# Performance work log

Measured on AMD Instinct MI355X. Metric: run time of the kernel, lower is better.

Reference implementation:

```python
import jax, jax.numpy as jnp
import numpy as np
import math

B, L_DEC, L_ENC, D, H = 2, 512, 2048, 1024, 16
HD = D // H
SCALE = HD ** -0.5
C = 5
N_TOP = min(L_DEC, max(1, int(C * math.log(L_DEC + 1))))      # 31
N_SAMPLE = min(L_ENC, max(1, int(C * math.log(L_ENC + 1))))   # 38
TAU = 1.0


def setup_inputs() -> dict:
    key = jax.random.key(0)
    ks = jax.random.split(key, 8)
    s = D ** -0.5
    return {
        "decoder_hidden": jax.random.normal(ks[0], (B, L_DEC, D), jnp.float32),
        "encoder_output": jax.random.normal(ks[1], (B, L_ENC, D), jnp.float32),
        "Wq": jax.random.normal(ks[2], (D, D), jnp.float32) * s,
        "Wk": jax.random.normal(ks[3], (D, D), jnp.float32) * s,
        "Wv": jax.random.normal(ks[4], (D, D), jnp.float32) * s,
        "Wo": jax.random.normal(ks[5], (D, D), jnp.float32) * s,
        "rms_w": jnp.ones((D,), jnp.float32),
        "alphas": 0.01 * jax.random.normal(ks[6], (6,), jnp.float32),
        "sample_idx": jax.random.permutation(ks[7], L_ENC)[:N_SAMPLE].astype(jnp.int32),
    }


def _split(x, L):
    # [B,L,D] -> [B,H,L,hd]
    return x.reshape(B, L, H, HD).transpose(0, 2, 1, 3)


def _merge(x):
    # [B,H,L,hd] -> [B,L,D]
    return x.transpose(0, 2, 1, 3).reshape(B, -1, D)


def _rmsnorm(x, w):
    return x * jax.lax.rsqrt(jnp.mean(x * x, axis=-1, keepdims=True) + 1e-6) * w


def _sdp(q, k, v):
    s = jnp.einsum('bhtd,bhsd->bhts', q, k) * SCALE
    return jnp.einsum('bhts,bhsd->bhtd', jax.nn.softmax(s, axis=-1), v)


def _linear(q, k, v):
    qf = jax.nn.elu(q * SCALE) + 1.0
    kf = jax.nn.elu(k) + 1.0
    kv = jnp.einsum('bhsd,bhsv->bhdv', kf, v)
    denom = jnp.maximum(jnp.einsum('bhtd,bhd->bht', qf, kf.sum(axis=2)), 1e-6)
    return jnp.einsum('bhtd,bhdv->bhtv', qf, kv) / denom[..., None]


def _cosine(q, k, v):
    qn = q / jnp.maximum(jnp.linalg.norm(q, axis=-1, keepdims=True), 1e-12)
    kn = k / jnp.maximum(jnp.linalg.norm(k, axis=-1, keepdims=True), 1e-12)
    qf = jax.nn.relu(qn) + 1e-6
    kf = jax.nn.relu(kn) + 1e-6
    kv = jnp.einsum('bhsd,bhsv->bhdv', kf, v)
    denom = jnp.maximum(jnp.einsum('bhtd,bhd->bht', qf, kf.sum(axis=2)), 1e-6)
    return jnp.einsum('bhtd,bhdv->bhtv', qf, kv) / denom[..., None]


def _probsparse(q, k, v, sample_idx):
    ks = k[:, :, sample_idx, :]                              # [B,H,n_sample,hd]
    qs = jnp.einsum('bhtd,bhsd->bhts', q, ks) * SCALE
    M = qs.max(axis=-1) - qs.mean(axis=-1)                   # sparsity score [B,H,T]
    _, top_idx = jax.lax.top_k(M, N_TOP)                     # [B,H,n_top]
    v_mean = v.mean(axis=2, keepdims=True)
    out = jnp.broadcast_to(v_mean, (B, H, L_DEC, HD))
    q_top = jnp.take_along_axis(q, top_idx[..., None], axis=2)
    s_top = jnp.einsum('bhtd,bhsd->bhts', q_top, k) * SCALE
    out_top = jnp.einsum('bhts,bhsd->bhtd', jax.nn.softmax(s_top, axis=-1), v)
    bi = jnp.arange(B)[:, None, None]
    hi = jnp.arange(H)[None, :, None]
    return out.at[bi, hi, top_idx].set(out_top)


def _local(q, k, v):
    W = max(4, int(L_ENC * 0.25))
    dec_pos = jnp.arange(L_DEC, dtype=jnp.float32)
    center = jnp.clip((dec_pos * (L_ENC / max(L_DEC, 1))).astype(jnp.int32), 0, L_ENC - 1)
    half = W // 2
    lo = jnp.clip(center - half, 0, L_ENC - 1)
    hi = jnp.clip(center + half, 0, L_ENC - 1)
    enc_pos = jnp.arange(L_ENC)
    mask = (enc_pos[None, :] >= lo[:, None]) & (enc_pos[None, :] <= hi[:, None])  # [T,S]
    s = jnp.einsum('bhtd,bhsd->bhts', q, k) * SCALE
    s = jnp.where(mask[None, None], s, -jnp.inf)
    attn = jax.nn.softmax(s, axis=-1)
    attn = jnp.where(jnp.isnan(attn), 1.0 / L_ENC, attn)
    return jnp.einsum('bhts,bhsd->bhtd', attn, v)


def _forward(decoder_hidden, encoder_output, Wq, Wk, Wv, Wo, rms_w, alphas, sample_idx):
    q = _split(decoder_hidden @ Wq, L_DEC)
    k = _split(encoder_output @ Wk, L_ENC)
    v = _split(encoder_output @ Wv, L_ENC)
    # MODES order: none, sdp, linear, probsparse, cosine, local
    branches = [_sdp(q, k, v), _linear(q, k, v), _probsparse(q, k, v, sample_idx),
                _cosine(q, k, v), _local(q, k, v)]
    w = jax.nn.softmax(alphas / TAU)
    out = w[0] * decoder_hidden  # 'none' branch is identity passthrough
    for i, raw in enumerate(branches):
        out = out + w[i + 1] * _rmsnorm(decoder_hidden + _merge(raw) @ Wo, rms_w)
    return out


def reference(decoder_hidden, encoder_output, Wq, Wk, Wv, Wo, rms_w, alphas, sample_idx):
    return _forward(decoder_hidden, encoder_output, Wq, Wk, Wv, Wo, rms_w, alphas, sample_idx)
```

## Files before the change

### kernel.cpp

```cpp
#include <hip/hip_runtime.h>
#include <math.h>

#define LDEC 512
#define LENC 2048
#define DMODEL 1024
#define NH 16
#define HD 64
#define SCALE 0.125f
#define NTOP 31
#define NSAMP 38

typedef __attribute__((ext_vector_type(8))) short bf16x8;
typedef __attribute__((ext_vector_type(4))) float f32x4;

__device__ inline float wave_sum(float v) {
#pragma unroll
  for (int m = 32; m > 0; m >>= 1) v += __shfl_xor(v, m);
  return v;
}

__device__ inline unsigned short f2bf(float x) {
  unsigned u = __float_as_uint(x);
  u += 0x7fff + ((u >> 16) & 1);
  return (unsigned short)(u >> 16);
}
__device__ inline float bf2f(unsigned short h) {
  return __uint_as_float(((unsigned)h) << 16);
}

__device__ __forceinline__ void gld16(const unsigned short* g, unsigned short* l) {
  __builtin_amdgcn_global_load_lds(
      (const __attribute__((address_space(1))) unsigned int*)g,
      (__attribute__((address_space(3))) unsigned int*)l, 16, 0, 0);
}

__device__ __forceinline__ int sws(int row, int col) {
  return row * 64 + (col ^ ((row & 7) << 3));
}

__global__ __launch_bounds__(256) void prologue(
    const float* __restrict__ dec, const float* __restrict__ enc,
    const float* __restrict__ Wq, const float* __restrict__ Wk,
    const float* __restrict__ Wv, const int* __restrict__ sidx,
    unsigned short* __restrict__ dh, unsigned short* __restrict__ dl,
    unsigned short* __restrict__ eh,
    unsigned short* __restrict__ Wqh, unsigned short* __restrict__ Wql,
    unsigned short* __restrict__ Wkh, unsigned short* __restrict__ Wvh,
    float* __restrict__ KsPart) {
  extern __shared__ char smraw[];
  int bx = blockIdx.x;
  int tid = threadIdx.x;
  if (bx < 5120) {
    int i = bx * 256 + tid;
    if (i < 262144) {
      float4 v = ((const float4*)dec)[i];
      ushort4 h = make_ushort4(f2bf(v.x), f2bf(v.y), f2bf(v.z), f2bf(v.w));
      ushort4 l = make_ushort4(f2bf(v.x - bf2f(h.x)), f2bf(v.y - bf2f(h.y)),
                               f2bf(v.z - bf2f(h.z)), f2bf(v.w - bf2f(h.w)));
      *(ushort4*)(dh + i * 4) = h;
      *(ushort4*)(dl + i * 4) = l;
    } else {
      int j = i - 262144;
      float4 v = ((const float4*)enc)[j];
      *(ushort4*)(eh + j * 4) =
          make_ushort4(f2bf(v.x), f2bf(v.y), f2bf(v.z), f2bf(v.w));
    }
  } else if (bx < 5888) {
    float (*t)[68] = (float(*)[68])smraw;
    int wb = bx - 5120;
    int which = wb >> 8, rem = wb & 255;
    const float* W = which == 0 ? Wq : (which == 1 ? Wk : Wv);
    unsigned short* Th = which == 0 ? Wqh : (which == 1 ? Wkh : Wvh);
    unsigned short* Tl = which == 0 ? Wql : nullptr;
    int k0 = (rem >> 4) * 64, n0 = (rem & 15) * 64;
#pragma unroll
    for (int i = 0; i < 4; ++i) {
      int c = tid + 256 * i;
      int r = c >> 4, c4 = (c & 15) * 4;
      float4 v = *(const float4*)(W + (size_t)(k0 + r) * DMODEL + n0 + c4);
      t[c4 + 0][r] = v.x; t[c4 + 1][r] = v.y; t[c4 + 2][r] = v.z; t[c4 + 3][r] = v.w;
    }
    __syncthreads();
#pragma unroll
    for (int i = 0; i < 4; ++i) {
      int c = tid + 256 * i;
      int n = c >> 4, k4 = (c & 15) * 4;
      float4 v = *(const float4*)&t[n][k4];
      ushort4 h = make_ushort4(f2bf(v.x), f2bf(v.y), f2bf(v.z), f2bf(v.w));
      *(ushort4*)(Th + (size_t)(n0 + n) * DMODEL + k0 + k4) = h;
      if (Tl) {
        ushort4 l = make_ushort4(f2bf(v.x - bf2f(h.x)), f2bf(v.y - bf2f(h.y)),
                                 f2bf(v.z - bf2f(h.z)), f2bf(v.w - bf2f(h.w)));
        *(ushort4*)(Tl + (size_t)(n0 + n) * DMODEL + k0 + k4) = l;
      }
    }
  } else {
    float* er = (float*)smraw;
    int sb = bx - 5888;
    int s = sb >> 5;
    int rem = sb & 31;
    int cchunk = rem >> 3, kc = rem & 7;
    int c = cchunk * 256 + tid;
    int srow = sidx[s];
    if (tid < 32) {
      int idx = tid * 4;
      *(float4*)&er[idx] =
          *(const float4*)(enc + (size_t)srow * DMODEL + kc * 128 + idx);
    }
    __syncthreads();
    float acc = 0.f;
    const float* wp = Wk + (size_t)(kc * 128) * DMODEL + c;
    for (int k0 = 0; k0 < 128; k0 += 16) {
      float w[16];
#pragma unroll
      for (int j = 0; j < 16; ++j) w[j] = wp[(size_t)(k0 + j) * DMODEL];
#pragma unroll
      for (int j = 0; j < 16; ++j) acc = fmaf(er[k0 + j], w[j], acc);
    }
    KsPart[(size_t)kc * (NSAMP * 1024) + s * 1024 + c] = acc;
  }
}

template <int BF16OUT>
__device__ __forceinline__ void gemm_epilogue(
    unsigned short* sm, f32x4 (&acc)[4][2], float* __restrict__ C,
    unsigned short* __restrict__ Cb, int row0, int col0, int wave, int lane) {
  const int l16 = lane & 15, quad = lane >> 4;
  float* eL = (float*)sm + wave * 576;
  const int rr = lane >> 2, cc = (lane & 3) * 8;
  const int wr = wave >> 2, wc = wave & 3;
#pragma unroll
  for (int x = 0; x < 4; ++x) {
#pragma unroll
    for (int y = 0; y < 2; ++y)
#pragma unroll
      for (int q = 0; q < 4; ++q)
        eL[(quad * 4 + q) * 36 + y * 16 + l16] = acc[x][y][q];
    float4 v0 = *(const float4*)&eL[rr * 36 + cc];
    float4 v1 = *(const float4*)&eL[rr * 36 + cc + 4];
    size_t ro = (size_t)(row0 + wr * 64 + x * 16 + rr) * DMODEL + col0 + wc * 32 + cc;
    if (BF16OUT) {
      uint2 o;
      o.x = (unsigned)f2bf(v0.x) | ((unsigned)f2bf(v0.y) << 16);
      o.y = (unsigned)f2bf(v0.z) | ((unsigned)f2bf(v0.w) << 16);
      *(uint2*)(Cb + ro) = o;
      o.x = (unsigned)f2bf(v1.x) | ((unsigned)f2bf(v1.y) << 16);
      o.y = (unsigned)f2bf(v1.z) | ((unsigned)f2bf(v1.w) << 16);
      *(uint2*)(Cb + ro + 4) = o;
    } else {
      *(float4*)(C + ro) = v0;
      *(float4*)(C + ro + 4) = v1;
    }
  }
}

template <int BF16OUT>
__device__ __forceinline__ void gemm512_1p_async(
    const unsigned short* __restrict__ Ah, const unsigned short* __restrict__ Bh,
    float* __restrict__ C, unsigned short* __restrict__ Cb, int row0, int col0) {
  extern __shared__ unsigned short sm[];
  const int BUFS = 16384;
  const int tid = threadIdx.x, lane = tid & 63, wave = tid >> 6;
  const int l16 = lane & 15, quad = lane >> 4;
  const int wr = wave >> 2, wc = wave & 3;

  const int srow = wave * 16 + (lane >> 3);
  const int scol = ((lane & 7) ^ (lane >> 3)) * 8;
  const unsigned short* gA = Ah + (size_t)(row0 + srow) * DMODEL + scol;
  const unsigned short* gB = Bh + (size_t)(col0 + srow) * DMODEL + scol;
  const int wofs = wave * 1024;

  f32x4 acc[4][2];
#pragma unroll
  for (int x = 0; x < 4; ++x)
#pragma unroll
    for (int y = 0; y < 2; ++y) acc[x][y] = (f32x4){0.f, 0.f, 0.f, 0.f};

  gld16(gA, sm + wofs);
  gld16(gA + (size_t)8 * DMODEL, sm + wofs + 512);
  gld16(gB, sm + 8192 + wofs);
  gld16(gB + (size_t)8 * DMODEL, sm + 8192 + wofs + 512);
  __syncthreads();

  for (int it = 0; it < 16; ++it) {
    const unsigned short* cur = sm + (it & 1) * BUFS;
    if (it < 15) {
      int ko = (it + 1) * 64;
      unsigned short* nxt = sm + ((it + 1) & 1) * BUFS;
      gld16(gA + ko, nxt + wofs);
      gld16(gA + (size_t)8 * DMODEL + ko, nxt + wofs + 512);
      gld16(gB + ko, nxt + 8192 + wofs);
      gld16(gB + (size_t)8 * DMODEL + ko, nxt + 8192 + wofs + 512);
    }
    bf16x8 a[2][4], b[2][2];
#pragma unroll
    for (int ks = 0; ks < 2; ++ks) {
#pragma unroll
      for (int x = 0; x < 4; ++x)
        a[ks][x] = *(const bf16x8*)&cur[sws(wr * 64 + x * 16 + l16, ks * 32 + quad * 8)];
#pragma unroll
      for (int y = 0; y < 2; ++y)
        b[ks][y] = *(const bf16x8*)&cur[8192 + sws(wc * 32 + y * 16 + l16, ks * 32 + quad * 8)];
    }
#pragma unroll
    for (int ks = 0; ks < 2; ++ks)
#pragma unroll
      for (int x = 0; x < 4; ++x)
#pragma unroll
        for (int y = 0; y < 2; ++y)
          acc[x][y] = __builtin_amdgcn_mfma_f32_16x16x32_bf16(a[ks][x], b[ks][y], acc[x][y], 0, 0, 0);
    __syncthreads();
  }
  gemm_epilogue<BF16OUT>(sm, acc, C, Cb, row0, col0, wave, lane);
}

__device__ __forceinline__ void gemm512_3p(
    const unsigned short* __restrict__ Ah, const unsigned short* __restrict__ Al,
    const unsigned short* __restrict__ Bh, const unsigned short* __restrict__ Bl,
    float* __restrict__ C, int row0, int col0) {
  extern __shared__ unsigned short sm[];
  const int BUFS = 20480;
  const int tid = threadIdx.x, lane = tid & 63, wave = tid >> 6;
  const int l16 = lane & 15, quad = lane >> 4;
  const int wr = wave >> 2, wc = wave & 3;

  const int r = tid >> 2, kc = tid & 3;
  const unsigned short* gAh = Ah + (size_t)(row0 + r) * DMODEL + kc * 8;
  const unsigned short* gBh = Bh + (size_t)(col0 + r) * DMODEL + kc * 8;
  const unsigned short* gAl = Al + (size_t)(row0 + r) * DMODEL + kc * 8;
  const unsigned short* gBl = Bl + (size_t)(col0 + r) * DMODEL + kc * 8;
  const int lofs = r * 40 + kc * 8;

  f32x4 acc[4][2];
#pragma unroll
  for (int x = 0; x < 4; ++x)
#pragma unroll
    for (int y = 0; y < 2; ++y) acc[x][y] = (f32x4){0.f, 0.f, 0.f, 0.f};

  uint4 pah = *(const uint4*)gAh, pbh = *(const uint4*)gBh;
  uint4 pal = *(const uint4*)gAl, pbl = *(const uint4*)gBl;
  *(uint4*)&sm[lofs] = pah;
  *(uint4*)&sm[5120 + lofs] = pbh;
  *(uint4*)&sm[10240 + lofs] = pal;
  *(uint4*)&sm[15360 + lofs] = pbl;
  pah = *(const uint4*)(gAh + 32);
  pbh = *(const uint4*)(gBh + 32);
  pal = *(const uint4*)(gAl + 32);
  pbl = *(const uint4*)(gBl + 32);
  __syncthreads();

  for (int it = 0; it < 32; ++it) {
    const unsigned short* cur = sm + (it & 1) * BUFS;
    bf16x8 ah[4], bh[2], al[4], bl[2];
#pragma unroll
    for (int x = 0; x < 4; ++x) {
      ah[x] = *(const bf16x8*)&cur[(wr * 64 + x * 16 + l16) * 40 + quad * 8];
      al[x] = *(const bf16x8*)&cur[10240 + (wr * 64 + x * 16 + l16) * 40 + quad * 8];
    }
#pragma unroll
    for (int y = 0; y < 2; ++y) {
      bh[y] = *(const bf16x8*)&cur[5120 + (wc * 32 + y * 16 + l16) * 40 + quad * 8];
      bl[y] = *(const bf16x8*)&cur[15360 + (wc * 32 + y * 16 + l16) * 40 + quad * 8];
    }
#pragma unroll
    for (int x = 0; x < 4; ++x)
#pragma unroll
      for (int y = 0; y < 2; ++y) {
        acc[x][y] = __builtin_amdgcn_mfma_f32_16x16x32_bf16(ah[x], bh[y], acc[x][y], 0, 0, 0);
        acc[x][y] = __builtin_amdgcn_mfma_f32_16x16x32_bf16(ah[x], bl[y], acc[x][y], 0, 0, 0);
        acc[x][y] = __builtin_amdgcn_mfma_f32_16x16x32_bf16(al[x], bh[y], acc[x][y], 0, 0, 0);
      }
    if (it < 31) {
// ... 99 lines not shown
      const int s0 = ch * 64;
      {
        const unsigned short* kr = Kg + (size_t)(s0 + sK) * DMODEL + d16;
        uint4 p0 = *(const uint4*)kr;
        uint4 p1 = *(const uint4*)(kr + 8);
        float kvv[16];
        kvv[0] = __uint_as_float(p0.x << 16);
        kvv[1] = __uint_as_float(p0.x & 0xffff0000u);
        kvv[2] = __uint_as_float(p0.y << 16);
        kvv[3] = __uint_as_float(p0.y & 0xffff0000u);
        kvv[4] = __uint_as_float(p0.z << 16);
        kvv[5] = __uint_as_float(p0.z & 0xffff0000u);
        kvv[6] = __uint_as_float(p0.w << 16);
        kvv[7] = __uint_as_float(p0.w & 0xffff0000u);
        kvv[8] = __uint_as_float(p1.x << 16);
        kvv[9] = __uint_as_float(p1.x & 0xffff0000u);
        kvv[10] = __uint_as_float(p1.y << 16);
        kvv[11] = __uint_as_float(p1.y & 0xffff0000u);
        kvv[12] = __uint_as_float(p1.z << 16);
        kvv[13] = __uint_as_float(p1.z & 0xffff0000u);
        kvv[14] = __uint_as_float(p1.w << 16);
        kvv[15] = __uint_as_float(p1.w & 0xffff0000u);
        float ss = 0.f;
#pragma unroll
        for (int j = 0; j < 16; ++j) ss = fmaf(kvv[j], kvv[j], ss);
        ss += __shfl_xor(ss, 1);
        ss += __shfl_xor(ss, 2);
        if ((tid & 3) == 0) nrm[sK] = sqrtf(ss);
#pragma unroll
        for (int j = 0; j < 16; ++j) Kt[sK][d16 + j] = kvv[j];
      }
#pragma unroll
      for (int i = 0; i < 4; ++i) {
        int sv = sVb + 16 * i;
        float4 vv = *(const float4*)(Vg + (size_t)(s0 + sv) * DMODEL + v4);
        vpart.x += vv.x; vpart.y += vv.y; vpart.z += vv.z; vpart.w += vv.w;
        unsigned short h0 = f2bf(vv.x), h1 = f2bf(vv.y);
        unsigned short h2 = f2bf(vv.z), h3 = f2bf(vv.w);
        Vu[sv][v4 + 0] = ((unsigned)h0 << 16) | (unsigned)f2bf(vv.x - bf2f(h0));
        Vu[sv][v4 + 1] = ((unsigned)h1 << 16) | (unsigned)f2bf(vv.y - bf2f(h1));
        Vu[sv][v4 + 2] = ((unsigned)h2 << 16) | (unsigned)f2bf(vv.z - bf2f(h2));
        Vu[sv][v4 + 3] = ((unsigned)h3 << 16) | (unsigned)f2bf(vv.w - bf2f(h3));
      }
      __syncthreads();
#pragma unroll
      for (int kk = 0; kk < 2; ++kk) {
        const int sb = kk * 32 + quad * 8;
        bf16x8 aLh, aLl, aCh, aCl;
#pragma unroll
        for (int j = 0; j < 8; ++j) {
          float kval = Kt[sb + j][dblk + l16];
          float nn = nrm[sb + j];
          float kfl = kval > 0.f ? kval + 1.f : __expf(kval);
          float kn = kval / fmaxf(nn, 1e-12f);
          float kfc = fmaxf(kn, 0.f) + 1e-6f;
          kslp += kfl;
          kscp += kfc;
          unsigned short hL = f2bf(kfl);
          aLh[j] = hL;
          aLl[j] = f2bf(kfl - bf2f(hL));
          unsigned short hC = f2bf(kfc);
          aCh[j] = hC;
          aCl[j] = f2bf(kfc - bf2f(hC));
        }
#pragma unroll
        for (int n = 0; n < 4; ++n) {
          bf16x8 bhv, blv;
#pragma unroll
          for (int j = 0; j < 8; ++j) {
            unsigned uv = Vu[sb + j][n * 16 + l16];
            bhv[j] = (short)(unsigned short)(uv >> 16);
            blv[j] = (short)(unsigned short)(uv & 0xffffu);
          }
          accL[n] = __builtin_amdgcn_mfma_f32_16x16x32_bf16(aLh, bhv, accL[n], 0, 0, 0);
          accL[n] = __builtin_amdgcn_mfma_f32_16x16x32_bf16(aLh, blv, accL[n], 0, 0, 0);
          accL[n] = __builtin_amdgcn_mfma_f32_16x16x32_bf16(aLl, bhv, accL[n], 0, 0, 0);
          accC[n] = __builtin_amdgcn_mfma_f32_16x16x32_bf16(aCh, bhv, accC[n], 0, 0, 0);
          accC[n] = __builtin_amdgcn_mfma_f32_16x16x32_bf16(aCh, blv, accC[n], 0, 0, 0);
          accC[n] = __builtin_amdgcn_mfma_f32_16x16x32_bf16(aCl, bhv, accC[n], 0, 0, 0);
        }
      }
      __syncthreads();
    }
    const int obase = part * 131072 + bh * 4096;
#pragma unroll
    for (int n = 0; n < 4; ++n)
#pragma unroll
      for (int q = 0; q < 4; ++q) {
        int o = obase + (dblk + quad * 4 + q) * 64 + n * 16 + l16;
        kvpL[o] = accL[n][q];
        kvpC[o] = accC[n][q];
      }
    kslp += __shfl_xor(kslp, 16);
    kslp += __shfl_xor(kslp, 32);
    kscp += __shfl_xor(kscp, 16);
    kscp += __shfl_xor(kscp, 32);
    if (quad == 0) {
      kspL[part * 2048 + bh * 64 + dblk + l16] = kslp;
      kspC[part * 2048 + bh * 64 + dblk + l16] = kscp;
    }
    vpart.x += __shfl_xor(vpart.x, 16); vpart.x += __shfl_xor(vpart.x, 32);
    vpart.y += __shfl_xor(vpart.y, 16); vpart.y += __shfl_xor(vpart.y, 32);
    vpart.z += __shfl_xor(vpart.z, 16); vpart.z += __shfl_xor(vpart.z, 32);
    vpart.w += __shfl_xor(vpart.w, 16); vpart.w += __shfl_xor(vpart.w, 32);
    if (quad == 0) vred[wv * 16 + l16] = vpart;
    __syncthreads();
    if (tid < 16) {
      float4 a0 = vred[tid], a1 = vred[16 + tid];
      float4 a2 = vred[32 + tid], a3 = vred[48 + tid];
      float4 s = make_float4(a0.x + a1.x + a2.x + a3.x, a0.y + a1.y + a2.y + a3.y,
                             a0.z + a1.z + a2.z + a3.z, a0.w + a1.w + a2.w + a3.w);
      *(float4*)&vsp[part * 2048 + bh * 64 + tid * 4] = s;
    }
  } else {
    float (*ksL)[65] = (float(*)[65])smraw;
    int bx = bx0 - 1536;
    int bh = bx >> 2, chunk = bx & 3;
    int b = bh >> 4, h = bh & 15;
    int t0 = chunk * 128;
    const float* Qb = Q + (b * LDEC) * DMODEL + h * HD;
    for (int slot = tid; slot < NSAMP * 16; slot += 256) {
      int r = slot >> 4, c4 = slot & 15;
      const float* kp = KsPart + r * 1024 + h * HD + c4 * 4;
      float4 kx = *(const float4*)kp;
#pragma unroll
      for (int p = 1; p < 8; ++p) {
        float4 k2 = *(const float4*)(kp + (size_t)p * (NSAMP * 1024));
        kx.x += k2.x; kx.y += k2.y; kx.z += k2.z; kx.w += k2.w;
      }
      ksL[r][c4 * 4 + 0] = kx.x; ksL[r][c4 * 4 + 1] = kx.y;
      ksL[r][c4 * 4 + 2] = kx.z; ksL[r][c4 * 4 + 3] = kx.w;
    }
    __syncthreads();
    if (tid < 128) {
      float qr[64];
      const float* qrow = Qb + (size_t)(t0 + tid) * DMODEL;
#pragma unroll
      for (int d4 = 0; d4 < 16; ++d4)
        *(float4*)&qr[d4 * 4] = *(const float4*)(qrow + d4 * 4);
      float mx = -INFINITY, sm = 0.f;
      for (int j = 0; j < NSAMP; ++j) {
        float s = 0.f;
#pragma unroll
        for (int d = 0; d < 64; ++d) s = fmaf(qr[d], ksL[j][d], s);
        s *= SCALE;
        mx = fmaxf(mx, s);
        sm += s;
      }
      Mout[bh * LDEC + t0 + tid] = mx - sm / (float)NSAMP;
    }
  }
}

__global__ __launch_bounds__(256) void tail2(
    const float* __restrict__ kvpL, const float* __restrict__ kvpC,
    const float* __restrict__ kspL, const float* __restrict__ kspC,
    const float* __restrict__ vsp, float* __restrict__ kvL,
    float* __restrict__ kvC, float* __restrict__ ksL,
    float* __restrict__ ksC, float* __restrict__ vmean,
    const float* __restrict__ Mbuf, int* __restrict__ sel) {
  extern __shared__ char smraw[];
  int bx = blockIdx.x;
  int tid = threadIdx.x;
  if (bx < 1048) {
    int i = bx * 256 + tid;
    if (i < 131072) {
      float s = 0.f;
#pragma unroll
      for (int p = 0; p < 16; ++p) s += kvpL[p * 131072 + i];
      kvL[i] = s;
    } else if (i < 262144) {
      int j = i - 131072;
      float s = 0.f;
#pragma unroll
      for (int p = 0; p < 16; ++p) s += kvpC[p * 131072 + j];
      kvC[j] = s;
    } else if (i < 268288) {
      int j = i - 262144;
      int which = j >> 11, jj = j & 2047;
      const float* src = which == 0 ? kspL : (which == 1 ? kspC : vsp);
      float s = 0.f;
#pragma unroll
      for (int p = 0; p < 16; ++p) s += src[p * 2048 + jj];
      if (which == 0) ksL[jj] = s;
      else if (which == 1) ksC[jj] = s;
      else vmean[jj] = s * (1.f / 2048.f);
    }
  } else {
    float* vals = (float*)smraw;
    int* flag = (int*)(smraw + 2048);
    float* wvs = (float*)(smraw + 4096);
    int* wis = (int*)(smraw + 4112);
    int bh = bx - 1048;
    int lane = tid & 63, g = tid >> 6;
    vals[tid] = Mbuf[bh * 512 + tid];
    vals[tid + 256] = Mbuf[bh * 512 + tid + 256];
    flag[tid] = 0; flag[tid + 256] = 0;
    __syncthreads();
    for (int it = 0; it < NTOP; ++it) {
      float v0 = vals[tid]; int i0 = tid;
      float v1 = vals[tid + 256];
      if (v1 > v0) { v0 = v1; i0 = tid + 256; }
#pragma unroll
      for (int mm = 32; mm > 0; mm >>= 1) {
        float ov = __shfl_xor(v0, mm);
        int oi = __shfl_xor(i0, mm);
        if (ov > v0 || (ov == v0 && oi < i0)) { v0 = ov; i0 = oi; }
      }
      if (lane == 0) { wvs[g] = v0; wis[g] = i0; }
      __syncthreads();
      if (tid == 0) {
        float bv = wvs[0]; int bi = wis[0];
#pragma unroll
        for (int w = 1; w < 4; ++w)
          if (wvs[w] > bv || (wvs[w] == bv && wis[w] < bi)) { bv = wvs[w]; bi = wis[w]; }
        vals[bi] = -INFINITY;
        flag[bi] = 1;
      }
      __syncthreads();
    }
    sel[bh * 512 + tid] = flag[tid];
    sel[bh * 512 + tid + 256] = flag[tid + 256];
  }
}

__global__ __launch_bounds__(256) void attn_mfma(
    const float* __restrict__ Qf, const unsigned short* __restrict__ Kb,
    const unsigned short* __restrict__ Vt,
    float* __restrict__ OsP0, float* __restrict__ OsP1,
    float* __restrict__ OsP2, float* __restrict__ OsP3,
    float* __restrict__ OlS0, float* __restrict__ OlS1,
    float* __restrict__ st) {
  __shared__ unsigned short Ks[2][4096];
  __shared__ unsigned short Vs[2][4096];
  __shared__ unsigned short Ps[4][1024];
  const int tid = threadIdx.x;
  const int wave = tid >> 6, lane = tid & 63;
  const int l16 = lane & 15, quad = lane >> 4;
  const int bx = blockIdx.x;
  const int xcd = bx & 7, sub = bx >> 3;
  const int qt = sub & 7, qr = (sub >> 3) & 3, grp = sub >> 5;
  const int bh = xcd + 8 * grp;
  const int b = bh >> 4, h = bh & 15;
  const int tbase = qt * 64 + wave * 16;
  const int sbase = qr * 512;

  const float* qrow = Qf + (size_t)(b * LDEC + tbase + l16) * DMODEL + h * HD + quad * 8;
  bf16x8 qa0, qa1;
  {
    float4 a0 = *(const float4*)qrow, a1 = *(const float4*)(qrow + 4);
    float4 a2 = *(const float4*)(qrow + 32), a3 = *(const float4*)(qrow + 36);
    qa0[0] = f2bf(a0.x * SCALE); qa0[1] = f2bf(a0.y * SCALE);
    qa0[2] = f2bf(a0.z * SCALE); qa0[3] = f2bf(a0.w * SCALE);
    qa0[4] = f2bf(a1.x * SCALE); qa0[5] = f2bf(a1.y * SCALE);
    qa0[6] = f2bf(a1.z * SCALE); qa0[7] = f2bf(a1.w * SCALE);
    qa1[0] = f2bf(a2.x * SCALE); qa1[1] = f2bf(a2.y * SCALE);
    qa1[2] = f2bf(a2.z * SCALE); qa1[3] = f2bf(a2.w * SCALE);
    qa1[4] = f2bf(a3.x * SCALE); qa1[5] = f2bf(a3.y * SCALE);
    qa1[6] = f2bf(a3.z * SCALE); qa1[7] = f2bf(a3.w * SCALE);
  }

  bf16x8 bone;
#pragma unroll
  for (int j = 0; j < 8; ++j) bone[j] = (short)0x3f80;

  int tA = tbase + l16;
  int cA = min(4 * tA, LENC - 1);
  int loA = max(cA - 256, 0), hiA = min(cA + 256, LENC - 1);
  const int loW = max(4 * tbase - 256, 0);
  const int hiW = min(4 * (tbase + 15) + 256, LENC - 1);
  const bool blockAny = (sbase <= hiW) && (sbase + 511 >= loW);

  f32x4 Os[4], Ol[4], Ssum, Slsum;
#pragma unroll
  for (int n = 0; n < 4; ++n) {
    Os[n] = (f32x4){0.f, 0.f, 0.f, 0.f};
    Ol[n] = (f32x4){0.f, 0.f, 0.f, 0.f};
  }
  Ssum = (f32x4){0.f, 0.f, 0.f, 0.f};
  Slsum = (f32x4){0.f, 0.f, 0.f, 0.f};

  const int c0 = tid, c1 = tid + 256;
  const unsigned short* kg0 = Kb + (size_t)(b * LENC + sbase + (c0 >> 3)) * DMODEL + h * HD + (c0 & 7) * 8;
  const unsigned short* kg1 = Kb + (size_t)(b * LENC + sbase + (c1 >> 3)) * DMODEL + h * HD + (c1 & 7) * 8;
  const unsigned short* vg0 = Vt + (size_t)(bh * 64 + (c0 >> 3)) * LENC + sbase + (c0 & 7) * 8;
  const unsigned short* vg1 = Vt + (size_t)(bh * 64 + (c1 >> 3)) * LENC + sbase + (c1 & 7) * 8;
  const int of0 = sws(c0 >> 3, (c0 & 7) * 8);
  const int of1 = sws(c1 >> 3, (c1 & 7) * 8);

  uint4 pk0, pk1, pv0, pv1;
  pk0 = *(const uint4*)kg0; pk1 = *(const uint4*)kg1;
  pv0 = *(const uint4*)vg0; pv1 = *(const uint4*)vg1;
  *(uint4*)&Ks[0][of0] = pk0; *(uint4*)&Ks[0][of1] = pk1;
  *(uint4*)&Vs[0][of0] = pv0; *(uint4*)&Vs[0][of1] = pv1;
  __syncthreads();

  for (int it = 0; it < 8; ++it) {
    const int cur = it & 1;
    const int s0 = sbase + it * 64;
    const bool anyL = (s0 <= hiW) && (s0 + 63 >= loW);
    if (it < 7) {
      pk0 = *(const uint4*)(kg0 + (size_t)(it + 1) * 64 * DMODEL);
      pk1 = *(const uint4*)(kg1 + (size_t)(it + 1) * 64 * DMODEL);
      pv0 = *(const uint4*)(vg0 + (it + 1) * 64);
      pv1 = *(const uint4*)(vg1 + (it + 1) * 64);
    }
    const unsigned short* K_ = Ks[cur];
    const unsigned short* V_ = Vs[cur];

    f32x4 S[4];
#pragma unroll
    for (int n = 0; n < 4; ++n) {
      bf16x8 bk0 = *(const bf16x8*)&K_[sws(n * 16 + l16, quad * 8)];
      bf16x8 bk1 = *(const bf16x8*)&K_[sws(n * 16 + l16, 32 + quad * 8)];
      f32x4 z = (f32x4){0.f, 0.f, 0.f, 0.f};
      z = __builtin_amdgcn_mfma_f32_16x16x32_bf16(qa0, bk0, z, 0, 0, 0);
      S[n] = __builtin_amdgcn_mfma_f32_16x16x32_bf16(qa1, bk1, z, 0, 0, 0);
    }

    unsigned short* Pw = Ps[wave];
#pragma unroll
    for (int n = 0; n < 4; ++n)
#pragma unroll
      for (int r = 0; r < 4; ++r)
        Pw[sws(quad * 4 + r, n * 16 + l16)] = f2bf(__expf(S[n][r]));
    bf16x8 aP0 = *(const bf16x8*)&Pw[sws(l16, quad * 8)];
    bf16x8 aP1 = *(const bf16x8*)&Pw[sws(l16, 32 + quad * 8)];
    Ssum = __builtin_amdgcn_mfma_f32_16x16x32_bf16(aP0, bone, Ssum, 0, 0, 0);
    Ssum = __builtin_amdgcn_mfma_f32_16x16x32_bf16(aP1, bone, Ssum, 0, 0, 0);
#pragma unroll
    for (int n = 0; n < 4; ++n) {
      bf16x8 bv0 = *(const bf16x8*)&V_[sws(n * 16 + l16, quad * 8)];
      bf16x8 bv1 = *(const bf16x8*)&V_[sws(n * 16 + l16, 32 + quad * 8)];
      Os[n] = __builtin_amdgcn_mfma_f32_16x16x32_bf16(aP0, bv0, Os[n], 0, 0, 0);
      Os[n] = __builtin_amdgcn_mfma_f32_16x16x32_bf16(aP1, bv1, Os[n], 0, 0, 0);
    }
    if (anyL) {
      bf16x8 aL0 = aP0, aL1 = aP1;
#pragma unroll
      for (int j = 0; j < 8; ++j) {
        int sc = s0 + quad * 8 + j;
        if (sc < loA || sc > hiA) aL0[j] = 0;
        if (sc + 32 < loA || sc + 32 > hiA) aL1[j] = 0;
      }
      Slsum = __builtin_amdgcn_mfma_f32_16x16x32_bf16(aL0, bone, Slsum, 0, 0, 0);
      Slsum = __builtin_amdgcn_mfma_f32_16x16x32_bf16(aL1, bone, Slsum, 0, 0, 0);
#pragma unroll
      for (int n = 0; n < 4; ++n) {
        bf16x8 bv0 = *(const bf16x8*)&V_[sws(n * 16 + l16, quad * 8)];
        bf16x8 bv1 = *(const bf16x8*)&V_[sws(n * 16 + l16, 32 + quad * 8)];
        Ol[n] = __builtin_amdgcn_mfma_f32_16x16x32_bf16(aL0, bv0, Ol[n], 0, 0, 0);
        Ol[n] = __builtin_amdgcn_mfma_f32_16x16x32_bf16(aL1, bv1, Ol[n], 0, 0, 0);
      }
    }
    if (it < 7) {
      unsigned short* KL = Ks[1 - cur];
      unsigned short* VL = Vs[1 - cur];
      *(uint4*)&KL[of0] = pk0; *(uint4*)&KL[of1] = pk1;
      *(uint4*)&VL[of0] = pv0; *(uint4*)&VL[of1] = pv1;
    }
    __syncthreads();
  }

  float* osp = qr == 0 ? OsP0 : (qr == 1 ? OsP1 : (qr == 2 ? OsP2 : OsP3));
  float* olp = (qr & 1) ? OlS1 : OlS0;
  float* sp = st + qr * 32768;
#pragma unroll
  for (int r = 0; r < 4; ++r) {
    int t = tbase + quad * 4 + r;
#pragma unroll
    for (int n = 0; n < 4; ++n) {
      size_t o = (size_t)(b * LDEC + t) * DMODEL + h * HD + n * 16 + l16;
      osp[o] = Os[n][r];
      if (blockAny) olp[o] = Ol[n][r];
    }
    if (l16 == 0) {
      int sr = bh * 512 + t;
      sp[sr] = Ssum[r];
      sp[16384 + sr] = Slsum[r];
    }
  }
}

__global__ __launch_bounds__(256) void combine_fill(
    const float* __restrict__ braw, const float* __restrict__ P1,
    const float* __restrict__ P2, const float* __restrict__ P3,
    const float* __restrict__ L1, const float* __restrict__ st,
    const float* __restrict__ vmean, const int* __restrict__ sel,
    const float* __restrict__ Q, const float* __restrict__ kvL,
    const float* __restrict__ kvC, const float* __restrict__ ksL,
    const float* __restrict__ ksC,
    unsigned short* __restrict__ b16, const float* __restrict__ Wo,
    unsigned short* __restrict__ Woh) {
  extern __shared__ char smraw[];
  __shared__ float sh[2][4][64];
  int bx0 = blockIdx.x;
  int tid = threadIdx.x;
  if (bx0 < 1024) {
    int i4 = bx0 * 256 + tid;
    int i = i4 * 4;
    int col = i & 1023, bt = i >> 10;
    int t = bt & 511, b = bt >> 9, h = col >> 6, d = col & 63;
    int bh = b * 16 + h;
    int sr = bh * 512 + t;
    float iS = 1.f / (st[sr] + st[32768 + sr] + st[65536 + sr] + st[98304 + sr]);
    float iL = 1.f / (st[16384 + sr] + st[49152 + sr] + st[81920 + sr] + st[114688 + sr]);
    float4 s0 = *(const float4*)(braw + i);
    float4 s1 = *(const float4*)(P1 + i);
    float4 s2 = *(const float4*)(P2 + i);
    float4 s3 = *(const float4*)(P3 + i);
    int c = min(4 * t, LENC - 1);
    int lo = max(c - 256, 0), hi = min(c + 256, LENC - 1);
    int q0 = lo >> 9, q1 = hi >> 9;
    const float* Lp0 = (q0 & 1) ? L1 : (braw + 4194304);
    float4 l = *(const float4*)(Lp0 + i);
    if (q1 != q0) {
      const float* Lp1 = (q1 & 1) ? L1 : (braw + 4194304);
      float4 l2 = *(const float4*)(Lp1 + i);
      l.x += l2.x; l.y += l2.y; l.z += l2.z; l.w += l2.w;
    }
    float4 os = make_float4((s0.x + s1.x + s2.x + s3.x) * iS,
                            (s0.y + s1.y + s2.y + s3.y) * iS,
                            (s0.z + s1.z + s2.z + s3.z) * iS,
                            (s0.w + s1.w + s2.w + s3.w) * iS);
    float4 ol = make_float4(l.x * iL, l.y * iL, l.z * iL, l.w * iL);
    float4 pp = sel[sr] ? os : *(const float4*)(vmean + bh * 64 + d);
    uint2 o2;
    o2.x = (unsigned)f2bf(os.x) | ((unsigned)f2bf(os.y) << 16);
    o2.y = (unsigned)f2bf(os.z) | ((unsigned)f2bf(os.w) << 16);
    *(uint2*)(b16 + i) = o2;
    o2.x = (unsigned)f2bf(pp.x) | ((unsigned)f2bf(pp.y) << 16);
    o2.y = (unsigned)f2bf(pp.z) | ((unsigned)f2bf(pp.w) << 16);
    *(uint2*)(b16 + 2097152 + i) = o2;
    o2.x = (unsigned)f2bf(ol.x) | ((unsigned)f2bf(ol.y) << 16);
    o2.y = (unsigned)f2bf(ol.z) | ((unsigned)f2bf(ol.w) << 16);
    *(uint2*)(b16 + 4194304 + i) = o2;
  } else if (bx0 < 5120) {
    int lane = tid & 63, g = tid >> 6;
    int row = (bx0 - 1024) * 4 + g;
    int bh = row >> 9, t = row & 511;
    int b = bh >> 4, h = bh & 15;
    float qv = Q[(b * LDEC + t) * DMODEL + h * HD + lane];
    float x = qv * SCALE;
    float qfl = x > 0.f ? x + 1.f : __expf(x);
    float qnorm = sqrtf(wave_sum(qv * qv));
    float qn = qv / fmaxf(qnorm, 1e-12f);
    float qfc = fmaxf(qn, 0.f) + 1e-6f;
    sh[0][g][lane] = qfl;
    sh[1][g][lane] = qfc;
    float denL = fmaxf(wave_sum(qfl * ksL[bh * 64 + lane]), 1e-6f);
    float denC = fmaxf(wave_sum(qfc * ksC[bh * 64 + lane]), 1e-6f);
    const float* kvLb = kvL + bh * 4096;
    const float* kvCb = kvC + bh * 4096;
    float aL = 0.f, aC = 0.f;
#pragma unroll
    for (int d = 0; d < 64; ++d) {
      aL = fmaf(sh[0][g][d], kvLb[d * 64 + lane], aL);
      aC = fmaf(sh[1][g][d], kvCb[d * 64 + lane], aC);
    }
    int o = (b * LDEC + t) * DMODEL + h * HD + lane;
    b16[1048576 + o] = f2bf(aL / denL);
    b16[3145728 + o] = f2bf(aC / denC);
  } else {
    float (*tl)[68] = (float(*)[68])smraw;
    int wb = bx0 - 5120;
    int k0 = (wb >> 4) * 64, n0 = (wb & 15) * 64;
#pragma unroll
    for (int i = 0; i < 4; ++i) {
      int c = tid + 256 * i;
      int r = c >> 4, c4 = (c & 15) * 4;
      float4 v = *(const float4*)(Wo + (size_t)(k0 + r) * DMODEL + n0 + c4);
      tl[c4 + 0][r] = v.x; tl[c4 + 1][r] = v.y; tl[c4 + 2][r] = v.z; tl[c4 + 3][r] = v.w;
    }
    __syncthreads();
#pragma unroll
    for (int i = 0; i < 4; ++i) {
      int c = tid + 256 * i;
      int n = c >> 4, k4 = (c & 15) * 4;
      float4 v = *(const float4*)&tl[n][k4];
      *(ushort4*)(Woh + (size_t)(n0 + n) * DMODEL + k0 + k4) =
          make_ushort4(f2bf(v.x), f2bf(v.y), f2bf(v.z), f2bf(v.w));
    }
  }
}

__global__ __launch_bounds__(256) void combine(
    const float* __restrict__ dec, const float* __restrict__ proj,
    const float* __restrict__ rmsw, const float* __restrict__ alphas,
    float* __restrict__ out) {
  __shared__ float red[4];
  int row = blockIdx.x;
  int tid = threadIdx.x, lane = tid & 63, g = tid >> 6;
  int base = row * DMODEL + tid * 4;
  float4 dv = *(const float4*)(dec + base);
  float4 wv = *(const float4*)(rmsw + tid * 4);
  float a[6];
  float amax = -INFINITY;
#pragma unroll
  for (int i = 0; i < 6; ++i) { a[i] = alphas[i]; amax = fmaxf(amax, a[i]); }
  float asum = 0.f;
#pragma unroll
  for (int i = 0; i < 6; ++i) { a[i] = __expf(a[i] - amax); asum += a[i]; }
#pragma unroll
  for (int i = 0; i < 6; ++i) a[i] /= asum;
  float4 acc = make_float4(a[0] * dv.x, a[0] * dv.y, a[0] * dv.z, a[0] * dv.w);
  for (int br = 0; br < 5; ++br) {
    float4 pv = *(const float4*)(proj + br * 1048576 + base);
    float4 xx = make_float4(dv.x + pv.x, dv.y + pv.y, dv.z + pv.z, dv.w + pv.w);
    float ssq = xx.x * xx.x + xx.y * xx.y + xx.z * xx.z + xx.w * xx.w;
    float wsum = wave_sum(ssq);
    if (lane == 0) red[g] = wsum;
    __syncthreads();
    float tot = red[0] + red[1] + red[2] + red[3];
    float rr = rsqrtf(tot / 1024.f + 1e-6f);
    float wb = a[br + 1];
    acc.x += wb * xx.x * rr * wv.x;
    acc.y += wb * xx.y * rr * wv.y;
    acc.z += wb * xx.z * rr * wv.z;
    acc.w += wb * xx.w * rr * wv.w;
    __syncthreads();
  }
  *(float4*)(out + base) = acc;
}

extern "C" void kernel_launch(void* const* d_in, const int* in_sizes, int n_in,
                              void* d_out, int out_size, void* d_ws, size_t ws_size,
                              hipStream_t stream) {
  const float* dec = (const float*)d_in[0];
  const float* enc = (const float*)d_in[1];
  const float* Wq = (const float*)d_in[2];
  const float* Wk = (const float*)d_in[3];
  const float* Wv = (const float*)d_in[4];
  const float* Wo = (const float*)d_in[5];
  const float* rmsw = (const float*)d_in[6];
  const float* alphas = (const float*)d_in[7];
  const int* sidx = (const int*)d_in[8];

  const size_t M = 1048576;
  float* ws = (float*)d_ws;
  float* Q    = ws;
  unsigned short* Kb16 = (unsigned short*)(ws + M);
  float* KsPart = ws + 3 * M;
  float* V    = ws + 5 * M;
  float* Vtb_f= ws + 9 * M;
  float* braw = ws + 11 * M;
  unsigned short* Wqh = (unsigned short*)(ws + 9 * M);
  unsigned short* Wql = (unsigned short*)(ws + 9 * M + M / 2);
  unsigned short* Wkh = (unsigned short*)(ws + 10 * M);
  unsigned short* Wvh = (unsigned short*)(ws + 10 * M + M / 2);
  unsigned short* eh  = (unsigned short*)(ws + 11 * M);
  unsigned short* dh  = (unsigned short*)(ws + 15 * M);
  unsigned short* dl  = (unsigned short*)(ws + 15 * M + M / 2);
  unsigned short* Vtb = (unsigned short*)Vtb_f;
  float* kvpL = ws + 11 * M;
  float* kvpC = ws + 13 * M;
  float* kspL = ws + 15 * M;
  float* kspC = ws + 15 * M + 32768;
  float* vsp  = ws + 15 * M + 65536;
  float* OsP1 = ws + 5 * M;
  float* OsP2 = ws + 3 * M;
  float* OsP3 = ws + 4 * M;
  float* OlS1 = ws + 6 * M;
  float* stats = ws + 7 * M;
  float* tail = ws + 16 * M;
  float* kvL  = tail;
  float* kvC  = tail + 131072;
  float* ksL  = tail + 262144;
  float* ksC  = tail + 264192;
  float* vmean= tail + 266240;
  float* Mbuf = tail + 317440;
  int*   sel  = (int*)(tail + 333824);
  unsigned short* braw16 = (unsigned short*)(ws + 12 * M);
  unsigned short* Woh = (unsigned short*)(ws + 14 * M + M / 2);
  float* proj = ws + 3 * M + M / 2;

  hipLaunchKernelGGL(prologue, dim3(7104), dim3(256), 17408, stream,
                     dec, enc, Wq, Wk, Wv, sidx, dh, dl, eh, Wqh, Wql, Wkh, Wvh, KsPart);
  hipLaunchKernelGGL(gemm_qkv, dim3(72, 8), dim3(512), 81920, stream,
                     dh, dl, Wqh, Wql, Q, eh, Wkh, Kb16, Wvh, V);
  hipLaunchKernelGGL(trio, dim3(1664), dim3(256), 34816, stream,
                     V, Vtb, Kb16, kvpL, kvpC, kspL, kspC, vsp, Q, KsPart, Mbuf);
  hipLaunchKernelGGL(tail2, dim3(1080), dim3(256), 4224, stream,
                     kvpL, kvpC, kspL, kspC, vsp, kvL, kvC, ksL, ksC, vmean, Mbuf, sel);
  hipLaunchKernelGGL(attn_mfma, dim3(1024), dim3(256), 0, stream, Q, Kb16, Vtb,
                     braw, OsP1, OsP2, OsP3, braw + 4 * M, OlS1, stats);
  hipLaunchKernelGGL(combine_fill, dim3(5376), dim3(256), 17408, stream,
                     braw, OsP1, OsP2, OsP3, OlS1, stats, vmean, sel,
                     Q, kvL, kvC, ksL, ksC, braw16, Wo, Woh);
  hipLaunchKernelGGL(gemm_one, dim3(40, 8), dim3(512), 65536, stream, braw16, Woh, proj);
  hipLaunchKernelGGL(combine, dim3(1024), dim3(256), 0, stream, dec, proj, rmsw, alphas,
                     (float*)d_out);
}
```

Baseline: 278.0 us.

## Merge tail2 into attention launch and move Wo conversion into prologue

The reduction/top-k work of tail2 now runs as extra blocks appended to the attn_mfma grid, removing one kernel launch and letting the small reductions overlap with attention. The Wo transpose-to-bf16 is moved from combine_fill into the prologue. Workspace buffers are relocated so attention partial outputs no longer alias the kvp partial sums that the merged blocks read concurrently. This adds a larger workspace footprint, and the merged blocks carry attn_mfma's static shared-memory allocation, which may reduce occupancy for those blocks.

```diff
diff --git a/kernel.cpp b/kernel.cpp
--- a/kernel.cpp
+++ b/kernel.cpp
@@ -46,7 +46,8 @@
     unsigned short* __restrict__ eh,
     unsigned short* __restrict__ Wqh, unsigned short* __restrict__ Wql,
     unsigned short* __restrict__ Wkh, unsigned short* __restrict__ Wvh,
-    float* __restrict__ KsPart) {
+    float* __restrict__ KsPart,
+    const float* __restrict__ Wo, unsigned short* __restrict__ Woh) {
   extern __shared__ char smraw[];
   int bx = blockIdx.x;
   int tid = threadIdx.x;
@@ -94,7 +95,7 @@
         *(ushort4*)(Tl + (size_t)(n0 + n) * DMODEL + k0 + k4) = l;
       }
     }
-  } else {
+  } else if (bx < 7104) {
     float* er = (float*)smraw;
     int sb = bx - 5888;
     int s = sb >> 5;
@@ -118,6 +119,26 @@
       for (int j = 0; j < 16; ++j) acc = fmaf(er[k0 + j], w[j], acc);
     }
     KsPart[(size_t)kc * (NSAMP * 1024) + s * 1024 + c] = acc;
+  } else {
+    float (*tl)[68] = (float(*)[68])smraw;
+    int wb = bx - 7104;
+    int k0 = (wb >> 4) * 64, n0 = (wb & 15) * 64;
+#pragma unroll
+    for (int i = 0; i < 4; ++i) {
+      int c = tid + 256 * i;
+      int r = c >> 4, c4 = (c & 15) * 4;
+      float4 v = *(const float4*)(Wo + (size_t)(k0 + r) * DMODEL + n0 + c4);
+      tl[c4 + 0][r] = v.x; tl[c4 + 1][r] = v.y; tl[c4 + 2][r] = v.z; tl[c4 + 3][r] = v.w;
+    }
+    __syncthreads();
+#pragma unroll
+    for (int i = 0; i < 4; ++i) {
+      int c = tid + 256 * i;
+      int n = c >> 4, k4 = (c & 15) * 4;
+      float4 v = *(const float4*)&tl[n][k4];
+      *(ushort4*)(Woh + (size_t)(n0 + n) * DMODEL + k0 + k4) =
+          make_ushort4(f2bf(v.x), f2bf(v.y), f2bf(v.z), f2bf(v.w));
+    }
   }
 }
 
@@ -523,92 +544,92 @@
   }
 }
 
-__global__ __launch_bounds__(256) void tail2(
+__global__ __launch_bounds__(256) void attn_mfma(
+    const float* __restrict__ Qf, const unsigned short* __restrict__ Kb,
+    const unsigned short* __restrict__ Vt,
+    float* __restrict__ OsP0, float* __restrict__ OsP1,
+    float* __restrict__ OsP2, float* __restrict__ OsP3,
+    float* __restrict__ OlS0, float* __restrict__ OlS1,
+    float* __restrict__ st,
     const float* __restrict__ kvpL, const float* __restrict__ kvpC,
     const float* __restrict__ kspL, const float* __restrict__ kspC,
     const float* __restrict__ vsp, float* __restrict__ kvL,
     float* __restrict__ kvC, float* __restrict__ ksL,
     float* __restrict__ ksC, float* __restrict__ vmean,
     const float* __restrict__ Mbuf, int* __restrict__ sel) {
-  extern __shared__ char smraw[];
-  int bx = blockIdx.x;
-  int tid = threadIdx.x;
-  if (bx < 1048) {
-    int i = bx * 256 + tid;
-    if (i < 131072) {
-      float s = 0.f;
-#pragma unroll
-      for (int p = 0; p < 16; ++p) s += kvpL[p * 131072 + i];
-      kvL[i] = s;
-    } else if (i < 262144) {
-      int j = i - 131072;
-      float s = 0.f;
-#pragma unroll
-      for (int p = 0; p < 16; ++p) s += kvpC[p * 131072 + j];
-      kvC[j] = s;
-    } else if (i < 268288) {
-      int j = i - 262144;
-      int which = j >> 11, jj = j & 2047;
-      const float* src = which == 0 ? kspL : (which == 1 ? kspC : vsp);
-      float s = 0.f;
-#pragma unroll
-      for (int p = 0; p < 16; ++p) s += src[p * 2048 + jj];
-      if (which == 0) ksL[jj] = s;
-      else if (which == 1) ksC[jj] = s;
-      else vmean[jj] = s * (1.f / 2048.f);
-    }
-  } else {
-    float* vals = (float*)smraw;
-    int* flag = (int*)(smraw + 2048);
-    float* wvs = (float*)(smraw + 4096);
-    int* wis = (int*)(smraw + 4112);
-    int bh = bx - 1048;
-    int lane = tid & 63, g = tid >> 6;
-    vals[tid] = Mbuf[bh * 512 + tid];
-    vals[tid + 256] = Mbuf[bh * 512 + tid + 256];
-    flag[tid] = 0; flag[tid + 256] = 0;
-    __syncthreads();
-    for (int it = 0; it < NTOP; ++it) {
-      float v0 = vals[tid]; int i0 = tid;
-      float v1 = vals[tid + 256];
-      if (v1 > v0) { v0 = v1; i0 = tid + 256; }
-#pragma unroll
-      for (int mm = 32; mm > 0; mm >>= 1) {
-        float ov = __shfl_xor(v0, mm);
-        int oi = __shfl_xor(i0, mm);
-        if (ov > v0 || (ov == v0 && oi < i0)) { v0 = ov; i0 = oi; }
-      }
-      if (lane == 0) { wvs[g] = v0; wis[g] = i0; }
-      __syncthreads();
-      if (tid == 0) {
-        float bv = wvs[0]; int bi = wis[0];
-#pragma unroll
-        for (int w = 1; w < 4; ++w)
-          if (wvs[w] > bv || (wvs[w] == bv && wis[w] < bi)) { bv = wvs[w]; bi = wis[w]; }
-        vals[bi] = -INFINITY;
-        flag[bi] = 1;
-      }
-      __syncthreads();
-    }
-    sel[bh * 512 + tid] = flag[tid];
-    sel[bh * 512 + tid + 256] = flag[tid + 256];
-  }
-}
-
-__global__ __launch_bounds__(256) void attn_mfma(
-    const float* __restrict__ Qf, const unsigned short* __restrict__ Kb,
-    const unsigned short* __restrict__ Vt,
-    float* __restrict__ OsP0, float* __restrict__ OsP1,
-    float* __restrict__ OsP2, float* __restrict__ OsP3,
-    float* __restrict__ OlS0, float* __restrict__ OlS1,
-    float* __restrict__ st) {
   __shared__ unsigned short Ks[2][4096];
   __shared__ unsigned short Vs[2][4096];
   __shared__ unsigned short Ps[4][1024];
   const int tid = threadIdx.x;
+  const int bxAll = blockIdx.x;
+  if (bxAll >= 1024) {
+    int bx = bxAll - 1024;
+    if (bx < 1048) {
+      int i = bx * 256 + tid;
+      if (i < 131072) {
+        float s = 0.f;
+#pragma unroll
+        for (int p = 0; p < 16; ++p) s += kvpL[p * 131072 + i];
+        kvL[i] = s;
+      } else if (i < 262144) {
+        int j = i - 131072;
+        float s = 0.f;
+#pragma unroll
+        for (int p = 0; p < 16; ++p) s += kvpC[p * 131072 + j];
+        kvC[j] = s;
+      } else if (i < 268288) {
+        int j = i - 262144;
+        int which = j >> 11, jj = j & 2047;
+        const float* src = which == 0 ? kspL : (which == 1 ? kspC : vsp);
+        float s = 0.f;
+#pragma unroll
+        for (int p = 0; p < 16; ++p) s += src[p * 2048 + jj];
+        if (which == 0) ksL[jj] = s;
+        else if (which == 1) ksC[jj] = s;
+        else vmean[jj] = s * (1.f / 2048.f);
+      }
+    } else {
+      char* smraw = (char*)Ks;
+      float* vals = (float*)smraw;
+      int* flag = (int*)(smraw + 2048);
+      float* wvs = (float*)(smraw + 4096);
+      int* wis = (int*)(smraw + 4112);
+      int bh = bx - 1048;
+      int lane = tid & 63, g = tid >> 6;
+      vals[tid] = Mbuf[bh * 512 + tid];
+      vals[tid + 256] = Mbuf[bh * 512 + tid + 256];
+      flag[tid] = 0; flag[tid + 256] = 0;
+      __syncthreads();
+      for (int it = 0; it < NTOP; ++it) {
+        float v0 = vals[tid]; int i0 = tid;
+        float v1 = vals[tid + 256];
+        if (v1 > v0) { v0 = v1; i0 = tid + 256; }
+#pragma unroll
+        for (int mm = 32; mm > 0; mm >>= 1) {
+          float ov = __shfl_xor(v0, mm);
+          int oi = __shfl_xor(i0, mm);
+          if (ov > v0 || (ov == v0 && oi < i0)) { v0 = ov; i0 = oi; }
+        }
+        if (lane == 0) { wvs[g] = v0; wis[g] = i0; }
+        __syncthreads();
+        if (tid == 0) {
+          float bv = wvs[0]; int bi = wis[0];
+#pragma unroll
+          for (int w = 1; w < 4; ++w)
+            if (wvs[w] > bv || (wvs[w] == bv && wis[w] < bi)) { bv = wvs[w]; bi = wis[w]; }
+          vals[bi] = -INFINITY;
+          flag[bi] = 1;
+        }
+        __syncthreads();
+      }
+      sel[bh * 512 + tid] = flag[tid];
+      sel[bh * 512 + tid + 256] = flag[tid + 256];
+    }
+    return;
+  }
   const int wave = tid >> 6, lane = tid & 63;
   const int l16 = lane & 15, quad = lane >> 4;
-  const int bx = blockIdx.x;
+  const int bx = bxAll;
   const int xcd = bx & 7, sub = bx >> 3;
   const int qt = sub & 7, qr = (sub >> 3) & 3, grp = sub >> 5;
   const int bh = xcd + 8 * grp;
@@ -754,16 +775,15 @@
 }
 
 __global__ __launch_bounds__(256) void combine_fill(
-    const float* __restrict__ braw, const float* __restrict__ P1,
+    const float* __restrict__ P0, const float* __restrict__ P1,
     const float* __restrict__ P2, const float* __restrict__ P3,
-    const float* __restrict__ L1, const float* __restrict__ st,
+    const float* __restrict__ L0, const float* __restrict__ L1,
+    const float* __restrict__ st,
     const float* __restrict__ vmean, const int* __restrict__ sel,
     const float* __restrict__ Q, const float* __restrict__ kvL,
     const float* __restrict__ kvC, const float* __restrict__ ksL,
     const float* __restrict__ ksC,
-    unsigned short* __restrict__ b16, const float* __restrict__ Wo,
-    unsigned short* __restrict__ Woh) {
-  extern __shared__ char smraw[];
+    unsigned short* __restrict__ b16) {
   __shared__ float sh[2][4][64];
   int bx0 = blockIdx.x;
   int tid = threadIdx.x;
@@ -776,17 +796,17 @@
     int sr = bh * 512 + t;
     float iS = 1.f / (st[sr] + st[32768 + sr] + st[65536 + sr] + st[98304 + sr]);
     float iL = 1.f / (st[16384 + sr] + st[49152 + sr] + st[81920 + sr] + st[114688 + sr]);
-    float4 s0 = *(const float4*)(braw + i);
+    float4 s0 = *(const float4*)(P0 + i);
     float4 s1 = *(const float4*)(P1 + i);
     float4 s2 = *(const float4*)(P2 + i);
     float4 s3 = *(const float4*)(P3 + i);
     int c = min(4 * t, LENC - 1);
     int lo = max(c - 256, 0), hi = min(c + 256, LENC - 1);
     int q0 = lo >> 9, q1 = hi >> 9;
-    const float* Lp0 = (q0 & 1) ? L1 : (braw + 4194304);
+    const float* Lp0 = (q0 & 1) ? L1 : L0;
     float4 l = *(const float4*)(Lp0 + i);
     if (q1 != q0) {
-      const float* Lp1 = (q1 & 1) ? L1 : (braw + 4194304);
+      const float* Lp1 = (q1 & 1) ? L1 : L0;
       float4 l2 = *(const float4*)(Lp1 + i);
       l.x += l2.x; l.y += l2.y; l.z += l2.z; l.w += l2.w;
     }
@@ -806,7 +826,7 @@
     o2.x = (unsigned)f2bf(ol.x) | ((unsigned)f2bf(ol.y) << 16);
     o2.y = (unsigned)f2bf(ol.z) | ((unsigned)f2bf(ol.w) << 16);
     *(uint2*)(b16 + 4194304 + i) = o2;
-  } else if (bx0 < 5120) {
+  } else {
     int lane = tid & 63, g = tid >> 6;
     int row = (bx0 - 1024) * 4 + g;
     int bh = row >> 9, t = row & 511;
@@ -832,26 +852,6 @@
     int o = (b * LDEC + t) * DMODEL + h * HD + lane;
     b16[1048576 + o] = f2bf(aL / denL);
     b16[3145728 + o] = f2bf(aC / denC);
-  } else {
-    float (*tl)[68] = (float(*)[68])smraw;
-    int wb = bx0 - 5120;
-    int k0 = (wb >> 4) * 64, n0 = (wb & 15) * 64;
-#pragma unroll
-    for (int i = 0; i < 4; ++i) {
-      int c = tid + 256 * i;
-      int r = c >> 4, c4 = (c & 15) * 4;
-      float4 v = *(const float4*)(Wo + (size_t)(k0 + r) * DMODEL + n0 + c4);
-      tl[c4 + 0][r] = v.x; tl[c4 + 1][r] = v.y; tl[c4 + 2][r] = v.z; tl[c4 + 3][r] = v.w;
-    }
-    __syncthreads();
-#pragma unroll
-    for (int i = 0; i < 4; ++i) {
-      int c = tid + 256 * i;
-      int n = c >> 4, k4 = (c & 15) * 4;
-      float4 v = *(const float4*)&tl[n][k4];
-      *(ushort4*)(Woh + (size_t)(n0 + n) * DMODEL + k0 + k4) =
-          make_ushort4(f2bf(v.x), f2bf(v.y), f2bf(v.z), f2bf(v.w));
-    }
   }
 }
 
@@ -914,7 +914,6 @@
   float* KsPart = ws + 3 * M;
   float* V    = ws + 5 * M;
   float* Vtb_f= ws + 9 * M;
-  float* braw = ws + 11 * M;
   unsigned short* Wqh = (unsigned short*)(ws + 9 * M);
   unsigned short* Wql = (unsigned short*)(ws + 9 * M + M / 2);
   unsigned short* Wkh = (unsigned short*)(ws + 10 * M);
@@ -928,11 +927,6 @@
   float* kspL = ws + 15 * M;
   float* kspC = ws + 15 * M + 32768;
   float* vsp  = ws + 15 * M + 65536;
-  float* OsP1 = ws + 5 * M;
-  float* OsP2 = ws + 3 * M;
-  float* OsP3 = ws + 4 * M;
-  float* OlS1 = ws + 6 * M;
-  float* stats = ws + 7 * M;
   float* tail = ws + 16 * M;
   float* kvL  = tail;
   float* kvC  = tail + 131072;
@@ -942,22 +936,30 @@
   float* Mbuf = tail + 317440;
   int*   sel  = (int*)(tail + 333824);
   unsigned short* braw16 = (unsigned short*)(ws + 12 * M);
-  unsigned short* Woh = (unsigned short*)(ws + 14 * M + M / 2);
+  unsigned short* Woh = (unsigned short*)(ws + 17 * M);
+  float* P0   = ws + 18 * M;
+  float* OsP1 = ws + 19 * M;
+  float* OsP2 = ws + 20 * M;
+  float* OsP3 = ws + 21 * M;
+  float* OlS0 = ws + 22 * M;
+  float* OlS1 = ws + 23 * M;
+  float* stats = ws + 24 * M;
   float* proj = ws + 3 * M + M / 2;
 
-  hipLaunchKernelGGL(prologue, dim3(7104), dim3(256), 17408, stream,
-                     dec, enc, Wq, Wk, Wv, sidx, dh, dl, eh, Wqh, Wql, Wkh, Wvh, KsPart);
+  hipLaunchKernelGGL(prologue, dim3(7360), dim3(256), 17408, stream,
+                     dec, enc, Wq, Wk, Wv, sidx, dh, dl, eh, Wqh, Wql, Wkh, Wvh,
+                     KsPart, Wo, Woh);
   hipLaunchKernelGGL(gemm_qkv, dim3(72, 8), dim3(512), 81920, stream,
                      dh, dl, Wqh, Wql, Q, eh, Wkh, Kb16, Wvh, V);
   hipLaunchKernelGGL(trio, dim3(1664), dim3(256), 34816, stream,
                      V, Vtb, Kb16, kvpL, kvpC, kspL, kspC, vsp, Q, KsPart, Mbuf);
-  hipLaunchKernelGGL(tail2, dim3(1080), dim3(256), 4224, stream,
-                     kvpL, kvpC, kspL, kspC, vsp, kvL, kvC, ksL, ksC, vmean, Mbuf, sel);
-  hipLaunchKernelGGL(attn_mfma, dim3(1024), dim3(256), 0, stream, Q, Kb16, Vtb,
-                     braw, OsP1, OsP2, OsP3, braw + 4 * M, OlS1, stats);
-  hipLaunchKernelGGL(combine_fill, dim3(5376), dim3(256), 17408, stream,
-                     braw, OsP1, OsP2, OsP3, OlS1, stats, vmean, sel,
-                     Q, kvL, kvC, ksL, ksC, braw16, Wo, Woh);
+  hipLaunchKernelGGL(attn_mfma, dim3(2104), dim3(256), 0, stream, Q, Kb16, Vtb,
+                     P0, OsP1, OsP2, OsP3, OlS0, OlS1, stats,
+                     kvpL, kvpC, kspL, kspC, vsp, kvL, kvC, ksL, ksC, vmean,
+                     Mbuf, sel);
+  hipLaunchKernelGGL(combine_fill, dim3(5120), dim3(256), 0, stream,
+                     P0, OsP1, OsP2, OsP3, OlS0, OlS1, stats, vmean, sel,
+                     Q, kvL, kvC, ksL, ksC, braw16);
   hipLaunchKernelGGL(gemm_one, dim3(40, 8), dim3(512), 65536, stream, braw16, Woh, proj);
   hipLaunchKernelGGL(combine, dim3(1024), dim3(256), 0, stream, dec, proj, rmsw, alphas,
                      (float*)d_out);
```

Measured after the change: 268.0 us. 1.04x faster.
